# Optimization experiments

Measured on AMD Instinct MI355X. Metric: run time of the kernel, lower is better.

Reference implementation:

```python
import jax, jax.numpy as jnp
import numpy as np

TEMPERATURE = 8.0

def _non_neg(x):
    # exp(x) for x<0, x+1 for x>=0 (non-negative feature map)
    return jnp.where(x < 0, jnp.exp(x), x + 1.0)

def setup_inputs() -> dict:
    key = jax.random.key(0)
    kq, kk, kv, km = jax.random.split(key, 4)
    B, H, S, D = 8, 16, 4096, 64
    q = jax.random.normal(kq, (B, H, S, D), dtype=jnp.float32)
    k = jax.random.normal(kk, (B, H, S, D), dtype=jnp.float32)
    v = jax.random.normal(kv, (B, H, S, D), dtype=jnp.float32)
    token_mask = jax.random.randint(km, (B, S), 0, 2).astype(bool)
    return {"q": q, "k": k, "v": v, "token_mask": token_mask}

def reference(q, k, v, token_mask):
    B, H, S, D = q.shape
    idx = jnp.arange(S, dtype=q.dtype)
    cos_vec = jnp.cos(jnp.pi / 2.0 / S * idx)[:, None]  # [S,1], broadcasts over D
    sin_vec = jnp.sin(jnp.pi / 2.0 / S * idx)[:, None]
    qf = _non_neg(q)
    kf = _non_neg(k)
    q_cos = qf * cos_vec
    q_sin = qf * sin_vec
    k_cos = kf * cos_vec
    k_sin = kf * sin_vec
    mask = token_mask[:, None, :, None].astype(q.dtype)  # [B,1,S,1]
    q_cos = q_cos * mask
    q_sin = q_sin * mask
    # global context: [B,H,D,Dv]
    k_cos_v = jnp.einsum('bhsd,bhse->bhde', k_cos, v)
    k_sin_v = jnp.einsum('bhsd,bhse->bhde', k_sin, v)
    values = (jnp.einsum('bhsd,bhde->bhse', q_cos, k_cos_v)
              + jnp.einsum('bhsd,bhde->bhse', q_sin, k_sin_v)) / TEMPERATURE
    return values
```

## Files before the change

kernel.cpp:

```cpp
#include <hip/hip_runtime.h>
#include <math.h>

#define Sn 4096
#define Dn 64
#define CW 3.834951969714103e-4f

typedef __attribute__((ext_vector_type(8)))  short short8;
typedef __attribute__((ext_vector_type(4)))  float f32x4;
typedef __attribute__((ext_vector_type(16))) float f32x16;

__device__ __forceinline__ unsigned int pack2(float lo, float hi) {
    unsigned int a = __float_as_uint(lo) + 0x8000u;
    unsigned int b = __float_as_uint(hi) + 0x8000u;
    return __builtin_amdgcn_perm(b, a, 0x07060302u);
}
__device__ __forceinline__ float nneg(float x) {
    return x < 0.f ? __expf(x) : x + 1.f;
}

__global__ __launch_bounds__(256) void k_init(float4* kv4, int* flag,
                                              const unsigned char* mask_raw) {
    int i = blockIdx.x * 256 + threadIdx.x;
    kv4[i] = make_float4(0.f, 0.f, 0.f, 0.f);
    if (blockIdx.x == 0) {
        __shared__ int s_any;
        if (threadIdx.x == 0) s_any = 0;
        __syncthreads();
        int any = 0;
        int base = threadIdx.x * 16;
        #pragma unroll
        for (int j = 0; j < 16; j++) {
            int idx = base + j;
            if ((idx & 3) && mask_raw[idx]) any = 1;
        }
        if (any) s_any = 1;
        __syncthreads();
        if (threadIdx.x == 0) *flag = s_any ? 0 : 1;
    }
}

__global__ __launch_bounds__(256, 4) void k_phase1(const float* __restrict__ kk,
                                                   const float* __restrict__ vv,
                                                   float* __restrict__ kv) {
    const int t    = threadIdx.x;
    const int bh   = blockIdx.x & 127;
    const int sblk = (blockIdx.x >> 7) << 9;
    const int lane = t & 63;
    const int w    = t >> 6;
    const int m    = lane & 31;
    const int sl   = lane >> 5;
    const int dt   = w >> 1;
    const int et   = w & 1;

    const float* kp = kk + (size_t)bh * (Sn * Dn) + (size_t)(sblk + sl * 8) * Dn + dt * 32 + m;
    const float* vp = vv + (size_t)bh * (Sn * Dn) + (size_t)(sblk + sl * 8) * Dn + et * 32 + m;

    const float CJT[8] = {1.0f,            0.999999926466f, 0.999999705859f, 0.999999338182f,
                          0.999998823452f, 0.999998161643f, 0.999997352766f, 0.999996396820f};
    const float SJT[8] = {0.0f,            3.83495188e-4f,  7.66989641e-4f,  1.15048534e-3f,
                          1.53398019e-3f,  1.91747478e-3f,  2.30096910e-3f,  2.68446310e-3f};

    f32x16 accC, accS;
    #pragma unroll
    for (int i = 0; i < 16; i++) { accC[i] = 0.f; accS[i] = 0.f; }

    float rk[2][8], rv[2][8];
    #pragma unroll
    for (int j = 0; j < 8; j++) {
        rk[0][j] = kp[j * Dn];
        rv[0][j] = vp[j * Dn];
    }
    const float sb0 = (float)(sblk + sl * 8);

    #pragma unroll 2
    for (int st = 0; st < 32; ++st) {
        const int cur = st & 1, nxt = cur ^ 1;
        if (st < 31) {
            const float* kq = kp + (size_t)(st + 1) * (16 * Dn);
            const float* vq = vp + (size_t)(st + 1) * (16 * Dn);
            #pragma unroll
            for (int j = 0; j < 8; j++) {
                rk[nxt][j] = kq[j * Dn];
                rv[nxt][j] = vq[j * Dn];
            }
        }
        float sa, ca;
        __sincosf(CW * (sb0 + (float)(st * 16)), &sa, &ca);
        union { unsigned int u[4]; short8 s; } Ac, As, Bv;
        #pragma unroll
        for (int jj = 0; jj < 4; jj++) {
            const float c0 = ca * CJT[2*jj]     - sa * SJT[2*jj];
            const float s0 = sa * CJT[2*jj]     + ca * SJT[2*jj];
            const float c1 = ca * CJT[2*jj + 1] - sa * SJT[2*jj + 1];
            const float s1 = sa * CJT[2*jj + 1] + ca * SJT[2*jj + 1];
            const float f0 = nneg(rk[cur][2*jj]);
            const float f1 = nneg(rk[cur][2*jj + 1]);
            Ac.u[jj] = pack2(f0 * c0, f1 * c1);
            As.u[jj] = pack2(f0 * s0, f1 * s1);
            Bv.u[jj] = pack2(rv[cur][2*jj], rv[cur][2*jj + 1]);
        }
        accC = __builtin_amdgcn_mfma_f32_32x32x16_bf16(Ac.s, Bv.s, accC, 0, 0, 0);
        accS = __builtin_amdgcn_mfma_f32_32x32x16_bf16(As.s, Bv.s, accS, 0, 0, 0);
    }

    float* base = kv + (size_t)bh * 8192;
    const int e = et * 32 + m;
    #pragma unroll
    for (int r = 0; r < 16; ++r) {
        const int d = dt * 32 + (r & 3) + 8 * (r >> 2) + 4 * sl;
        atomicAdd(base +        d * 64 + e, accC[r]);
        atomicAdd(base + 4096 + d * 64 + e, accS[r]);
    }
}

__global__ __launch_bounds__(256) void k_phase2(const float* __restrict__ qq,
                                                const void* __restrict__ mask_raw,
                                                const float* __restrict__ kv,
                                                const int* __restrict__ flag,
                                                float* __restrict__ out) {
    const int t    = threadIdx.x;
    const int bh   = blockIdx.x & 127;
    const int sblk = (blockIdx.x >> 7) << 9;
    const int b    = bh >> 4;
    const int lane = t & 63;
    const int w    = t >> 6;
    const int n    = lane & 15;
    const int q4   = lane >> 4;
    const int iflag = *flag;

    const float* kvb = kv + (size_t)bh * 8192;
    short8 Bc[4][2], Bs[4][2];
    #pragma unroll
    for (int et = 0; et < 4; et++) {
        const int e = et * 16 + n;
        #pragma unroll
        for (int ks = 0; ks < 2; ks++) {
            const int d0 = ks * 32 + q4 * 8;
            union { unsigned int u[4]; short8 s; } uc, us;
            #pragma unroll
            for (int jj = 0; jj < 4; jj++) {
                float c0 = kvb[(size_t)(d0 + 2 * jj)     * 64 + e];
                float c1 = kvb[(size_t)(d0 + 2 * jj + 1) * 64 + e];
                float s0 = kvb[4096 + (size_t)(d0 + 2 * jj)     * 64 + e];
                float s1 = kvb[4096 + (size_t)(d0 + 2 * jj + 1) * 64 + e];
                uc.u[jj] = pack2(c0, c1);
                us.u[jj] = pack2(s0, s1);
            }
            Bc[et][ks] = uc.s;
            Bs[et][ks] = us.s;
        }
    }

    const float* qb = qq + (size_t)bh * (Sn * Dn);
    float* ob       = out + (size_t)bh * (Sn * Dn);
    const unsigned char* m8 = (const unsigned char*)mask_raw;
    const int* m32          = (const int*)mask_raw;

    float4 pq[2][4];
    float  pmv[2];
    {
        int s_row = sblk + w * 16 + n;
        const float* qp = qb + (size_t)s_row * Dn + q4 * 8;
        pq[0][0] = *(const float4*)(qp);
        pq[0][1] = *(const float4*)(qp + 4);
        pq[0][2] = *(const float4*)(qp + 32);
        pq[0][3] = *(const float4*)(qp + 36);
        pmv[0] = iflag ? (m32[b * Sn + s_row] ? 1.f : 0.f)
                       : (m8 [b * Sn + s_row] ? 1.f : 0.f);
    }

    #pragma unroll 2
    for (int strip = 0; strip < 8; strip++) {
        const int cur = strip & 1, nxt = cur ^ 1;
        const int s_base = sblk + strip * 64 + w * 16;
        const int s_row  = s_base + n;
        float cs, snv;
        __sincosf(CW * (float)s_row, &snv, &cs);
        cs *= pmv[cur]; snv *= pmv[cur];
        float f[16];
        f[0]  = nneg(pq[cur][0].x); f[1]  = nneg(pq[cur][0].y);
        f[2]  = nneg(pq[cur][0].z); f[3]  = nneg(pq[cur][0].w);
        f[4]  = nneg(pq[cur][1].x); f[5]  = nneg(pq[cur][1].y);
        f[6]  = nneg(pq[cur][1].z); f[7]  = nneg(pq[cur][1].w);
        f[8]  = nneg(pq[cur][2].x); f[9]  = nneg(pq[cur][2].y);
        f[10] = nneg(pq[cur][2].z); f[11] = nneg(pq[cur][2].w);
        f[12] = nneg(pq[cur][3].x); f[13] = nneg(pq[cur][3].y);
        f[14] = nneg(pq[cur][3].z); f[15] = nneg(pq[cur][3].w);
        union { unsigned int u[4]; short8 s; } ac0, as0, ac1, as1;
        #pragma unroll
        for (int j = 0; j < 4; j++) {
            ac0.u[j] = pack2(f[2*j]     * cs,  f[2*j + 1]     * cs);
            as0.u[j] = pack2(f[2*j]     * snv, f[2*j + 1]     * snv);
            ac1.u[j] = pack2(f[8 + 2*j] * cs,  f[8 + 2*j + 1] * cs);
            as1.u[j] = pack2(f[8 + 2*j] * snv, f[8 + 2*j + 1] * snv);
        }
        if (strip < 7) {
            int s_row2 = sblk + (strip + 1) * 64 + w * 16 + n;
            const float* qp = qb + (size_t)s_row2 * Dn + q4 * 8;
            pq[nxt][0] = *(const float4*)(qp);
            pq[nxt][1] = *(const float4*)(qp + 4);
            pq[nxt][2] = *(const float4*)(qp + 32);
            pq[nxt][3] = *(const float4*)(qp + 36);
            pmv[nxt] = iflag ? (m32[b * Sn + s_row2] ? 1.f : 0.f)
                             : (m8 [b * Sn + s_row2] ? 1.f : 0.f);
        }
        f32x4 acc[4];
        #pragma unroll
        for (int et = 0; et < 4; et++) acc[et] = (f32x4){0.f, 0.f, 0.f, 0.f};
        #pragma unroll
        for (int et = 0; et < 4; et++) {
            acc[et] = __builtin_amdgcn_mfma_f32_16x16x32_bf16(ac0.s, Bc[et][0], acc[et], 0, 0, 0);
            acc[et] = __builtin_amdgcn_mfma_f32_16x16x32_bf16(ac1.s, Bc[et][1], acc[et], 0, 0, 0);
            acc[et] = __builtin_amdgcn_mfma_f32_16x16x32_bf16(as0.s, Bs[et][0], acc[et], 0, 0, 0);
            acc[et] = __builtin_amdgcn_mfma_f32_16x16x32_bf16(as1.s, Bs[et][1], acc[et], 0, 0, 0);
        }
        #pragma unroll
        for (int et = 0; et < 4; et++) {
            #pragma unroll
            for (int r = 0; r < 4; r++) {
                int row = q4 * 4 + r;
                __builtin_nontemporal_store(acc[et][r] * 0.125f,
                    ob + (size_t)(s_base + row) * 64 + et * 16 + n);
            }
        }
    }
}

extern "C" void kernel_launch(void* const* d_in, const int* in_sizes, int n_in,
                              void* d_out, int out_size, void* d_ws, size_t ws_size,
                              hipStream_t stream) {
    const float* q = (const float*)d_in[0];
    const float* k = (const float*)d_in[1];
    const float* v = (const float*)d_in[2];
    const void* mask = d_in[3];
    int*   flag = (int*)d_ws;
    float* kv   = (float*)((char*)d_ws + 256);

    k_init  <<<1024, 256, 0, stream>>>((float4*)kv, flag, (const unsigned char*)mask);
    k_phase1<<<1024, 256, 0, stream>>>(k, v, kv);
    k_phase2<<<1024, 256, 0, stream>>>(q, mask, kv, flag, (float*)d_out);
}
```

Before: 421.6 us.

## Stage K/V tiles through padded LDS with float4 loads in phase1

```diff
diff --git a/kernel.cpp b/kernel.cpp
--- a/kernel.cpp
+++ b/kernel.cpp
@@ -4,6 +4,7 @@
 #define Sn 4096
 #define Dn 64
 #define CW 3.834951969714103e-4f
+#define LP 68
 
 typedef __attribute__((ext_vector_type(8)))  short short8;
 typedef __attribute__((ext_vector_type(4)))  float f32x4;
@@ -42,6 +43,7 @@
 __global__ __launch_bounds__(256, 4) void k_phase1(const float* __restrict__ kk,
                                                    const float* __restrict__ vv,
                                                    float* __restrict__ kv) {
+    __shared__ float lds[2][2][32 * LP];
     const int t    = threadIdx.x;
     const int bh   = blockIdx.x & 127;
     const int sblk = (blockIdx.x >> 7) << 9;
@@ -52,8 +54,25 @@
     const int dt   = w >> 1;
     const int et   = w & 1;
 
-    const float* kp = kk + (size_t)bh * (Sn * Dn) + (size_t)(sblk + sl * 8) * Dn + dt * 32 + m;
-    const float* vp = vv + (size_t)bh * (Sn * Dn) + (size_t)(sblk + sl * 8) * Dn + et * 32 + m;
+    const float* kb = kk + (size_t)bh * (Sn * Dn);
+    const float* vb = vv + (size_t)bh * (Sn * Dn);
+
+    const int r0 = t >> 4;
+    const int c0 = (t & 15) * 4;
+
+#define LOADT(P, ti) do {                                                     \
+        pk[P][0] = *(const float4*)(kb + (size_t)(sblk + (ti) * 32 + r0) * 64 + c0);      \
+        pv[P][0] = *(const float4*)(vb + (size_t)(sblk + (ti) * 32 + r0) * 64 + c0);      \
+        pk[P][1] = *(const float4*)(kb + (size_t)(sblk + (ti) * 32 + 16 + r0) * 64 + c0); \
+        pv[P][1] = *(const float4*)(vb + (size_t)(sblk + (ti) * 32 + 16 + r0) * 64 + c0); \
+    } while (0)
+
+#define WRITET(B, P) do {                                                     \
+        *(float4*)&lds[B][0][r0 * LP + c0]        = pk[P][0];                 \
+        *(float4*)&lds[B][1][r0 * LP + c0]        = pv[P][0];                 \
+        *(float4*)&lds[B][0][(16 + r0) * LP + c0] = pk[P][1];                 \
+        *(float4*)&lds[B][1][(16 + r0) * LP + c0] = pv[P][1];                 \
+    } while (0)
 
     const float CJT[8] = {1.0f,            0.999999926466f, 0.999999705859f, 0.999999338182f,
                           0.999998823452f, 0.999998161643f, 0.999997352766f, 0.999996396820f};
@@ -64,44 +83,54 @@
     #pragma unroll
     for (int i = 0; i < 16; i++) { accC[i] = 0.f; accS[i] = 0.f; }
 
-    float rk[2][8], rv[2][8];
-    #pragma unroll
-    for (int j = 0; j < 8; j++) {
-        rk[0][j] = kp[j * Dn];
-        rv[0][j] = vp[j * Dn];
-    }
-    const float sb0 = (float)(sblk + sl * 8);
+    float4 pk[2][2], pv[2][2];
+    LOADT(0, 0);
+    WRITET(0, 0);
+    LOADT(1, 1);
+    asm volatile("s_waitcnt lgkmcnt(0)" ::: "memory");
+    __builtin_amdgcn_s_barrier();
 
     #pragma unroll 2
-    for (int st = 0; st < 32; ++st) {
-        const int cur = st & 1, nxt = cur ^ 1;
-        if (st < 31) {
-            const float* kq = kp + (size_t)(st + 1) * (16 * Dn);
-            const float* vq = vp + (size_t)(st + 1) * (16 * Dn);
-            #pragma unroll
-            for (int j = 0; j < 8; j++) {
-                rk[nxt][j] = kq[j * Dn];
-                rv[nxt][j] = vq[j * Dn];
-            }
-        }
-        float sa, ca;
-        __sincosf(CW * (sb0 + (float)(st * 16)), &sa, &ca);
-        union { unsigned int u[4]; short8 s; } Ac, As, Bv;
-        #pragma unroll
-        for (int jj = 0; jj < 4; jj++) {
-            const float c0 = ca * CJT[2*jj]     - sa * SJT[2*jj];
-            const float s0 = sa * CJT[2*jj]     + ca * SJT[2*jj];
-            const float c1 = ca * CJT[2*jj + 1] - sa * SJT[2*jj + 1];
-            const float s1 = sa * CJT[2*jj + 1] + ca * SJT[2*jj + 1];
-            const float f0 = nneg(rk[cur][2*jj]);
-            const float f1 = nneg(rk[cur][2*jj + 1]);
-            Ac.u[jj] = pack2(f0 * c0, f1 * c1);
-            As.u[jj] = pack2(f0 * s0, f1 * s1);
-            Bv.u[jj] = pack2(rv[cur][2*jj], rv[cur][2*jj + 1]);
-        }
-        accC = __builtin_amdgcn_mfma_f32_32x32x16_bf16(Ac.s, Bv.s, accC, 0, 0, 0);
-        accS = __builtin_amdgcn_mfma_f32_32x32x16_bf16(As.s, Bv.s, accS, 0, 0, 0);
-    }
+    for (int ti = 0; ti < 16; ++ti) {
+        const int cur = ti & 1, nxt = cur ^ 1;
+        if (ti < 15) WRITET(nxt, nxt);
+        if (ti < 14) LOADT(cur, ti + 2);
+        const float* Kt = &lds[cur][0][0];
+        const float* Vt = &lds[cur][1][0];
+        #pragma unroll
+        for (int ks = 0; ks < 2; ++ks) {
+            const int sloc = ks * 16 + sl * 8;
+            const int kbase = sloc * LP + dt * 32 + m;
+            const int vbase = sloc * LP + et * 32 + m;
+            float kf[8], vf[8];
+            #pragma unroll
+            for (int j = 0; j < 8; ++j) {
+                kf[j] = Kt[kbase + j * LP];
+                vf[j] = Vt[vbase + j * LP];
+            }
+            float sa, ca;
+            __sincosf(CW * (float)(sblk + ti * 32 + sloc), &sa, &ca);
+            union { unsigned int u[4]; short8 s; } Ac, As, Bv;
+            #pragma unroll
+            for (int jj = 0; jj < 4; ++jj) {
+                const float c0 = ca * CJT[2*jj]     - sa * SJT[2*jj];
+                const float s0 = sa * CJT[2*jj]     + ca * SJT[2*jj];
+                const float c1 = ca * CJT[2*jj + 1] - sa * SJT[2*jj + 1];
+                const float s1 = sa * CJT[2*jj + 1] + ca * SJT[2*jj + 1];
+                const float f0 = nneg(kf[2*jj]);
+                const float f1 = nneg(kf[2*jj + 1]);
+                Ac.u[jj] = pack2(f0 * c0, f1 * c1);
+                As.u[jj] = pack2(f0 * s0, f1 * s1);
+                Bv.u[jj] = pack2(vf[2*jj], vf[2*jj + 1]);
+            }
+            accC = __builtin_amdgcn_mfma_f32_32x32x16_bf16(Ac.s, Bv.s, accC, 0, 0, 0);
+            accS = __builtin_amdgcn_mfma_f32_32x32x16_bf16(As.s, Bv.s, accS, 0, 0, 0);
+        }
+        asm volatile("s_waitcnt lgkmcnt(0)" ::: "memory");
+        __builtin_amdgcn_s_barrier();
+    }
+#undef LOADT
+#undef WRITET
 
     float* base = kv + (size_t)bh * 8192;
     const int e = et * 32 + m;
```

New measurement: 462.9 us. 9.8% more time.
